# Kernel tuning notes

Measured on AMD Instinct MI355X. Metric: run time of the kernel, lower is better.

The kernel has to match this reference:

```python
import jax, jax.numpy as jnp
import numpy as np

VAR_FLOOR = 0.002
BS, A, IN, H, L, NNH, ATT, NACT = 1024, 32, 96, 64, 16, 64, 32, 16


def _lin(x, w, b):
    return x @ w.T + b


def _lrelu(x):
    return jax.nn.leaky_relu(x, 0.01)


def setup_inputs() -> dict:
    key = jax.random.key(0)
    ks = jax.random.split(key, 24)
    def w(k, o, i):
        return jax.random.normal(k, (o, i), jnp.float32) / np.float32(np.sqrt(i))
    def b(k, o):
        return jax.random.normal(k, (o,), jnp.float32) * 0.01
    N = BS * A
    return {
        "inputs": jax.random.normal(ks[0], (N, IN), jnp.float32),
        "hidden_state": jax.random.normal(ks[1], (N, H), jnp.float32),
        "eps": jax.random.normal(ks[2], (N, A * L), jnp.float32),
        "fc1_w": w(ks[3], H, IN), "fc1_b": b(ks[4], H),
        "gru_wih": w(ks[5], 3 * H, H), "gru_whh": w(ks[6], 3 * H, H),
        "gru_bih": b(ks[7], 3 * H), "gru_bhh": b(ks[8], 3 * H),
        "fc2_w": w(ks[9], NACT, H), "fc2_b": b(ks[10], NACT),
        "emb_w1": w(ks[11], NNH, H), "emb_b1": b(ks[12], NNH),
        "bn_g": jnp.ones((NNH,), jnp.float32), "bn_b": jnp.zeros((NNH,), jnp.float32),
        "emb_w2": w(ks[13], A * L * 2, NNH), "emb_b2": b(ks[14], A * L * 2),
        "msg_w1": w(ks[15], NNH, H + L), "msg_b1": b(ks[16], NNH),
        "msg_w2": w(ks[17], NACT, NNH), "msg_b2": b(ks[18], NACT),
        "wq_w": w(ks[19], ATT, H), "wq_b": b(ks[20], ATT),
        "wk_w": w(ks[21], ATT, L), "wk_b": b(ks[22], ATT),
        "bs": BS, "t": 0,
    }


def reference(inputs, hidden_state, eps, fc1_w, fc1_b, gru_wih, gru_whh, gru_bih,
              gru_bhh, fc2_w, fc2_b, emb_w1, emb_b1, bn_g, bn_b, emb_w2, emb_b2,
              msg_w1, msg_b1, msg_w2, msg_b2, wq_w, wq_b, wk_w, wk_b, bs, t):
    Hd = fc1_w.shape[0]
    x = jax.nn.relu(_lin(inputs, fc1_w, fc1_b))
    h_in = hidden_state.reshape(-1, Hd)
    # GRUCell
    gi = _lin(x, gru_wih, gru_bih)
    gh = _lin(h_in, gru_whh, gru_bhh)
    ir, iz, inn = jnp.split(gi, 3, axis=-1)
    hr, hz, hn = jnp.split(gh, 3, axis=-1)
    r = jax.nn.sigmoid(ir + hr)
    z = jax.nn.sigmoid(iz + hz)
    n = jnp.tanh(inn + r * hn)
    h = (1.0 - z) * n + z * h_in
    q = _lin(h, fc2_w, fc2_b)
    # embed_net: Linear -> BatchNorm(train) -> LeakyReLU -> Linear
    z1 = _lin(h, emb_w1, emb_b1)
    z1 = bn_g * (z1 - z1.mean(0)) / jnp.sqrt(z1.var(0) + 1e-5) + bn_b
    lat_par = _lin(_lrelu(z1), emb_w2, emb_b2)
    D = lat_par.shape[-1] // 2
    Ld = wk_w.shape[1]
    Ag = D // Ld
    mu = lat_par[:, :D]
    var = jnp.clip(jnp.exp(lat_par[:, D:]), VAR_FLOOR, None)
    latent = (mu + jnp.sqrt(var) * eps).reshape(bs, Ag, Ag, Ld)  # [b,i,j,L]
    # msg_net on (h of receiver j, latent[b,i,j])
    h3 = h.reshape(bs, Ag, Hd)
    h_rep = jnp.broadcast_to(h3[:, None, :, :], (bs, Ag, Ag, Hd))  # [b,i,j]=h[b,j]
    msg_in = jnp.concatenate([h_rep, latent], axis=-1)
    msg = _lin(_lrelu(_lin(msg_in, msg_w1, msg_b1)), msg_w2, msg_b2)  # (b,A,A,n_act)
    # attention gating
    att = wq_w.shape[0]
    query = _lin(h, wq_w, wq_b).reshape(bs, Ag, att) / np.float32(np.sqrt(att))
    key_ = _lin(latent, wk_w, wk_b)  # (b,A,A,att)
    alpha = jnp.einsum('bia,bija->bij', query, key_)
    alpha = jnp.where(jnp.eye(Ag, dtype=bool)[None], -1e9, alpha)
    alpha = jax.nn.softmax(alpha, axis=-1)
    agg = jnp.einsum('bij,bijn->bjn', alpha, msg)  # sum gated msgs over sender i
    return_q = q + agg.reshape(bs * Ag, -1)
    return (return_q, h)
```

## Files before the change

kernel.cpp:

```cpp
#include <hip/hip_runtime.h>
#include <math.h>

namespace {

constexpr int NROW = 32768;
constexpr int HDIM = 64;
constexpr int DH   = 512;

typedef __attribute__((ext_vector_type(8))) short bf16x8;
typedef __attribute__((ext_vector_type(4))) float f32x4;
typedef __attribute__((ext_vector_type(4))) unsigned uint4e;
typedef __attribute__((ext_vector_type(2))) unsigned uint2e;

__device__ __forceinline__ float sigmoidf_(float x) { return 1.f / (1.f + __expf(-x)); }
__device__ __forceinline__ float lrelu_(float x) { return x > 0.f ? x : 0.01f * x; }
__device__ __forceinline__ unsigned pkbf(float a, float b) {
  unsigned ua = __float_as_uint(a) + 0x8000u;
  unsigned ub = __float_as_uint(b) + 0x8000u;
  return __builtin_amdgcn_perm(ub, ua, 0x07060302);
}

__global__ __launch_bounds__(512, 1) void k_fgru(
    const float* __restrict__ in,
    const float* __restrict__ hprev,
    const float* __restrict__ fc1w, const float* __restrict__ fc1b,
    const float* __restrict__ wih, const float* __restrict__ whh,
    const float* __restrict__ bih, const float* __restrict__ bhh,
    const float* __restrict__ fc2w, const float* __restrict__ fc2b,
    const float* __restrict__ wqw, const float* __restrict__ wkw,
    const float* __restrict__ ew1, const float* __restrict__ eb1,
    float* __restrict__ qT, float* __restrict__ qkT, float* __restrict__ z1T,
    float* __restrict__ part, float* __restrict__ hout) {
  __shared__ char smem[91648];
  const int t = threadIdx.x;
  const int n0 = blockIdx.x * 128;
  short*    xS = (short*)smem;
  unsigned* gU = (unsigned*)(smem + 18432);
  float*    trF = (float*)(smem + 18432);
  unsigned* wU = (unsigned*)(smem + 73728);
  float*    sp1 = (float*)(smem + 87552);
  float*    sp2 = (float*)(smem + 89600);
  const float qs = 0.17677669529663687f;

  const float2* wih2 = (const float2*)wih;
  const float2* whh2 = (const float2*)whh;
  {
    float2 wv[12];
#pragma unroll
    for (int i = 0; i < 12; ++i) {
      int idx = t + 512 * i;
      int row = idx >> 5, kp = idx & 31;
      wv[i] = wih2[row * 32 + kp];
    }
#pragma unroll
    for (int i = 0; i < 12; ++i) {
      int idx = t + 512 * i;
      int row = idx >> 5, kp = idx & 31;
      int gate = row >> 6, cl = row & 63;
      gU[(gate * 64 + cl) * 36 + kp] = pkbf(wv[i].x, wv[i].y);
    }
#pragma unroll
    for (int i = 0; i < 12; ++i) {
      int idx = t + 512 * i;
      int row = idx >> 5, kp = idx & 31;
      wv[i] = whh2[row * 32 + kp];
    }
#pragma unroll
    for (int i = 0; i < 12; ++i) {
      int idx = t + 512 * i;
      int row = idx >> 5, kp = idx & 31;
      int gate = row >> 6, cl = row & 63;
      gU[((gate + 3) * 64 + cl) * 36 + kp] = pkbf(wv[i].x, wv[i].y);
    }
  }
  {
    float2 wv[5];
#pragma unroll
    for (int i = 0; i < 5; ++i) {
      int idx = t + 512 * i;
      int kp = idx & 31, cl = idx >> 5;
      const float* src = (cl < 16) ? (fc2w + cl * 64) : (ew1 + (cl - 16) * 64);
      wv[i] = *(const float2*)(src + 2 * kp);
    }
#pragma unroll
    for (int i = 0; i < 5; ++i) {
      int idx = t + 512 * i;
      int kp = idx & 31, cl = idx >> 5;
      int dst = (cl < 16) ? cl : (cl + 16);
      wU[dst * 36 + kp] = pkbf(wv[i].x, wv[i].y);
    }
  }
  {
    int kp = t & 31, row = t >> 5;
    float s0 = 0.f, s1 = 0.f;
#pragma unroll
    for (int a = 0; a < 32; ++a) {
      float wk = wkw[a * 16 + row];
      s0 = fmaf(wk, wqw[a * 64 + 2 * kp], s0);
      s1 = fmaf(wk, wqw[a * 64 + 2 * kp + 1], s1);
    }
    wU[(16 + row) * 36 + kp] = pkbf(s0 * qs, s1 * qs);
  }

  const int w = t >> 6, l = t & 63;
  const int m = l & 15, g = l >> 4;
  const int rowA = n0 + w * 16 + m;

  bf16x8 af[3];
#pragma unroll
  for (int ks = 0; ks < 3; ++ks) {
    const float4* p = (const float4*)(in + (size_t)rowA * 96 + ks * 32 + g * 8);
    float4 a = p[0], b = p[1];
    union { unsigned u[4]; bf16x8 h; } tw;
    tw.u[0] = pkbf(a.x, a.y); tw.u[1] = pkbf(a.z, a.w);
    tw.u[2] = pkbf(b.x, b.y); tw.u[3] = pkbf(b.z, b.w);
    af[ks] = tw.h;
  }
  {
    f32x4 accx[4];
#pragma unroll
    for (int ct = 0; ct < 4; ++ct) accx[ct] = (f32x4){0.f, 0.f, 0.f, 0.f};
#pragma unroll
    for (int ct = 0; ct < 4; ++ct)
#pragma unroll
      for (int ks = 0; ks < 3; ++ks) {
        const float4* p = (const float4*)(fc1w + (ct * 16 + m) * 96 + ks * 32 + g * 8);
        float4 a = p[0], b = p[1];
        union { unsigned u[4]; bf16x8 h; } tw;
        tw.u[0] = pkbf(a.x, a.y); tw.u[1] = pkbf(a.z, a.w);
        tw.u[2] = pkbf(b.x, b.y); tw.u[3] = pkbf(b.z, b.w);
        accx[ct] = __builtin_amdgcn_mfma_f32_16x16x32_bf16(af[ks], tw.h, accx[ct], 0, 0, 0);
      }
#pragma unroll
    for (int ct = 0; ct < 4; ++ct) {
      int c = ct * 16 + m;
      float bc = fc1b[c];
#pragma unroll
      for (int reg = 0; reg < 4; ++reg) {
        int nl = w * 16 + g * 4 + reg;
        float v = fmaxf(accx[ct][reg] + bc, 0.f);
        xS[nl * 72 + c] = (short)((__float_as_uint(v) + 0x8000u) >> 16);
      }
    }
  }
  __syncthreads();

  bf16x8 ax[2], ah[2];
#pragma unroll
  for (int ks = 0; ks < 2; ++ks) {
    ax[ks] = *(const bf16x8*)(xS + (w * 16 + m) * 72 + ks * 32 + g * 8);
    const float4* p = (const float4*)(hprev + (size_t)rowA * 64 + ks * 32 + g * 8);
    float4 a = p[0], b = p[1];
    union { unsigned u[4]; bf16x8 h; } tw;
    tw.u[0] = pkbf(a.x, a.y); tw.u[1] = pkbf(a.z, a.w);
    tw.u[2] = pkbf(b.x, b.y); tw.u[3] = pkbf(b.z, b.w);
    ah[ks] = tw.h;
  }
  const short* gS = (const short*)gU;
  float hc[4][4];
#pragma unroll 1
  for (int ct = 0; ct < 4; ++ct) {
    f32x4 a_ir = (f32x4){0.f,0.f,0.f,0.f}, a_iz = (f32x4){0.f,0.f,0.f,0.f},
          a_in = (f32x4){0.f,0.f,0.f,0.f}, a_hr = (f32x4){0.f,0.f,0.f,0.f},
          a_hz = (f32x4){0.f,0.f,0.f,0.f}, a_hn = (f32x4){0.f,0.f,0.f,0.f};
    int crow = ct * 16 + m;
#pragma unroll
    for (int ks = 0; ks < 2; ++ks) {
      bf16x8 b0 = *(const bf16x8*)(gS + (0 * 64 + crow) * 72 + ks * 32 + g * 8);
      bf16x8 b1 = *(const bf16x8*)(gS + (1 * 64 + crow) * 72 + ks * 32 + g * 8);
      bf16x8 b2 = *(const bf16x8*)(gS + (2 * 64 + crow) * 72 + ks * 32 + g * 8);
      bf16x8 b3 = *(const bf16x8*)(gS + (3 * 64 + crow) * 72 + ks * 32 + g * 8);
      bf16x8 b4 = *(const bf16x8*)(gS + (4 * 64 + crow) * 72 + ks * 32 + g * 8);
      bf16x8 b5 = *(const bf16x8*)(gS + (5 * 64 + crow) * 72 + ks * 32 + g * 8);
      a_ir = __builtin_amdgcn_mfma_f32_16x16x32_bf16(ax[ks], b0, a_ir, 0, 0, 0);
      a_iz = __builtin_amdgcn_mfma_f32_16x16x32_bf16(ax[ks], b1, a_iz, 0, 0, 0);
      a_in = __builtin_amdgcn_mfma_f32_16x16x32_bf16(ax[ks], b2, a_in, 0, 0, 0);
      a_hr = __builtin_amdgcn_mfma_f32_16x16x32_bf16(ah[ks], b3, a_hr, 0, 0, 0);
      a_hz = __builtin_amdgcn_mfma_f32_16x16x32_bf16(ah[ks], b4, a_hz, 0, 0, 0);
      a_hn = __builtin_amdgcn_mfma_f32_16x16x32_bf16(ah[ks], b5, a_hn, 0, 0, 0);
    }
    float bir = bih[crow], biz = bih[64 + crow], bin = bih[128 + crow];
    float bhr = bhh[crow], bhz = bhh[64 + crow], bhn = bhh[128 + crow];
#pragma unroll
    for (int reg = 0; reg < 4; ++reg) {
      int nl = w * 16 + g * 4 + reg;
      float hv = hprev[(size_t)(n0 + nl) * 64 + crow];
      float r  = sigmoidf_(a_ir[reg] + bir + a_hr[reg] + bhr);
      float z  = sigmoidf_(a_iz[reg] + biz + a_hz[reg] + bhz);
      float nn = tanhf(a_in[reg] + bin + r * (a_hn[reg] + bhn));
      hc[ct][reg] = (1.f - z) * nn + z * hv;
    }
  }
#pragma unroll
  for (int ct = 0; ct < 4; ++ct)
#pragma unroll
    for (int reg = 0; reg < 4; ++reg) {
      int nl = w * 16 + g * 4 + reg;
      xS[nl * 72 + ct * 16 + m] =
          (short)((__float_as_uint(hc[ct][reg]) + 0x8000u) >> 16);
    }

  bf16x8 af2[2];
#pragma unroll
  for (int ks = 0; ks < 2; ++ks)
    af2[ks] = *(const bf16x8*)(xS + (w * 16 + m) * 72 + ks * 32 + g * 8);
  const short* sW = (const short*)wU;
  f32x4 acc[6];
#pragma unroll
  for (int ct = 0; ct < 6; ++ct) acc[ct] = (f32x4){0.f, 0.f, 0.f, 0.f};
#pragma unroll
  for (int ct = 0; ct < 6; ++ct)
#pragma unroll
    for (int ks = 0; ks < 2; ++ks) {
      bf16x8 bw = *(const bf16x8*)(sW + (ct * 16 + m) * 72 + ks * 32 + g * 8);
      acc[ct] = __builtin_amdgcn_mfma_f32_16x16x32_bf16(af2[ks], bw, acc[ct], 0, 0, 0);
    }

  __syncthreads();
#pragma unroll
  for (int ct = 0; ct < 4; ++ct)
#pragma unroll
    for (int reg = 0; reg < 4; ++reg)
      trF[(ct * 16 + m) * 133 + w * 16 + g * 4 + reg] = hc[ct][reg];
  __syncthreads();
#pragma unroll
  for (int i = 0; i < 16; ++i) {
    int idx = t + 512 * i;
    int c = idx & 63, nl = idx >> 6;
    hout[(size_t)(n0 + nl) * 64 + c] = trF[c * 133 + nl];
  }

  float s1[4], s2[4];
#pragma unroll
  for (int zt = 0; zt < 4; ++zt) { s1[zt] = 0.f; s2[zt] = 0.f; }
  {
    int nb = n0 + w * 16 + g * 4;
    {
      float bc = fc2b[m];
      f32x4 v;
#pragma unroll
      for (int reg = 0; reg < 4; ++reg) v[reg] = acc[0][reg] + bc;
      *(f32x4*)(qT + (size_t)m * NROW + nb) = v;
    }
    *(f32x4*)(qkT + (size_t)m * NROW + nb) = acc[1];
#pragma unroll
    for (int ct = 2; ct < 6; ++ct) {
      int z = (ct - 2) * 16 + m;
      float bc = eb1[z];
      f32x4 v;
#pragma unroll
      for (int reg = 0; reg < 4; ++reg) {
        float zv = acc[ct][reg] + bc;
        v[reg] = zv;
        s1[ct - 2] += zv;
        s2[ct - 2] = fmaf(zv, zv, s2[ct - 2]);
      }
      *(f32x4*)(z1T + (size_t)z * NROW + nb) = v;
    }
  }
#pragma unroll
  for (int zt = 0; zt < 4; ++zt) {
    s1[zt] += __shfl_down(s1[zt], 16, 64);
    s1[zt] += __shfl_down(s1[zt], 32, 64);
    s2[zt] += __shfl_down(s2[zt], 16, 64);
    s2[zt] += __shfl_down(s2[zt], 32, 64);
  }
  if (l < 16) {
#pragma unroll
    for (int zt = 0; zt < 4; ++zt) {
      sp1[w * 64 + zt * 16 + m] = s1[zt];
      sp2[w * 64 + zt * 16 + m] = s2[zt];
    }
  }
  __syncthreads();
  if (t < 64) {
    float a1 = 0.f, a2 = 0.f;
#pragma unroll
    for (int k = 0; k < 8; ++k) {
      a1 += sp1[k * 64 + t];
      a2 += sp2[k * 64 + t];
    }
    part[(size_t)blockIdx.x * 128 + t] = a1;
    part[(size_t)blockIdx.x * 128 + 64 + t] = a2;
  }
}

__global__ __launch_bounds__(256) void k_bnstat(const float* __restrict__ part,
    const float* __restrict__ bng, const float* __restrict__ bnb,
    const float* __restrict__ ew2,
    float* __restrict__ stat, unsigned* __restrict__ ew2b) {
  if (blockIdx.x == 0) {
    __shared__ float red[512];
    const int t = threadIdx.x;
    const int c = t & 63, q = t >> 6;
    float s1 = 0.f, s2 = 0.f;
#pragma unroll 4
    for (int b = q; b < 256; b += 4) {
      s1 += part[(size_t)b * 128 + c];
      s2 += part[(size_t)b * 128 + 64 + c];
    }
    red[q * 64 + c] = s1;
    red[256 + q * 64 + c] = s2;
    __syncthreads();
    if (t < 64) {
      float a1 = red[t] + red[64 + t] + red[128 + t] + red[192 + t];
      float a2 = red[256 + t] + red[320 + t] + red[384 + t] + red[448 + t];
      float mean = a1 * (1.f / NROW);
      float var = a2 * (1.f / NROW) - mean * mean;
      float rstd = rsqrtf(var + 1e-5f);
      float sc = bng[t] * rstd;
      stat[t] = sc;
      stat[64 + t] = bnb[t] - mean * sc;
    }
  } else {
    const int rb = blockIdx.x - 1;
    const int t = threadIdx.x;
#pragma unroll
    for (int it = 0; it < 2; ++it) {
      int id2 = t + 256 * it;
      int r = rb * 16 + (id2 >> 5);
      int cp = id2 & 31;
      float2 v = *(const float2*)(ew2 + (size_t)r * 64 + 2 * cp);
      ew2b[(size_t)r * 32 + cp] = pkbf(v.x, v.y);
    }
  }
}

constexpr int LATB_OFF = 0;
constexpr int H3B_OFF  = 36864;
constexpr int W1H_OFF  = 41728;
constexpr int W1L_OFF  = 51456;
constexpr int W2P_OFF  = 54016;
constexpr int ALL_OFF  = 56448;
constexpr int MT_OFF   = 60672;
constexpr int QKL_OFF  = MT_OFF + 4864;
__global__ __launch_bounds__(512, 1) void k_msg(
    const unsigned* __restrict__ ew2b, const float* __restrict__ stat,
    const float* __restrict__ z1T, const float* __restrict__ eb2,
    const float* __restrict__ eps,
    const float* __restrict__ qkT,
    const float* __restrict__ qT, const float* __restrict__ hrow,
    const float* __restrict__ w1, const float* __restrict__ b1,
    const float* __restrict__ w2, const float* __restrict__ b2,
    float* __restrict__ out) {
  __shared__ char smem[81152];
  const int t = threadIdx.x;
  const int b = blockIdx.x;
  const int b32 = b * 32;
  unsigned* latB_dw = (unsigned*)(smem + LATB_OFF);

  const int w = t >> 6, l = t & 63;
  const int m = l & 15, g = l >> 4;

  {
    short* xz = (short*)(smem + MT_OFF);
    float zv[4];
#pragma unroll
    for (int it = 0; it < 4; ++it) {
      int idx = t + 512 * it;
      int i = idx & 31, c = idx >> 5;
      zv[it] = z1T[(size_t)c * NROW + b32 + i];
    }
#pragma unroll
    for (int it = 0; it < 4; ++it) {
      int idx = t + 512 * it;
      int i = idx & 31, c = idx >> 5;
      float v = lrelu_(fmaf(stat[c], zv[it], stat[64 + c]));
      xz[i * 76 + c] = (short)((__float_as_uint(v) + 0x8000u) >> 16);
    }
  }
  {
    float* qkL = (float*)(smem + QKL_OFF);
    int i = t & 31, ll = t >> 5;
    qkL[i * 20 + ll] = qkT[(size_t)ll * NROW + b32 + i];
  }
  {
    int cp = t & 31, jbase = t >> 5;
    const float2* h2 = (const float2*)hrow;
    float2 hv[2];
#pragma unroll
    for (int it = 0; it < 2; ++it)
      hv[it] = h2[((size_t)(b32 + jbase + 16 * it) * 64 + 2 * cp) >> 1];
    unsigned* dst = (unsigned*)(smem + H3B_OFF);
#pragma unroll
    for (int it = 0; it < 2; ++it)
      dst[(jbase + 16 * it) * 38 + cp] = pkbf(hv[it].x, hv[it].y);
  }
  {
    int kp = t & 31, cb = t >> 5;
    const float2* w12 = (const float2*)w1;
    float2 wv[4];
#pragma unroll
    for (int it = 0; it < 4; ++it)
      wv[it] = w12[((cb + 16 * it) * 80 + 2 * kp) >> 1];
    unsigned* dst = (unsigned*)(smem + W1H_OFF);
#pragma unroll
    for (int it = 0; it < 4; ++it)
      dst[(cb + 16 * it) * 38 + kp] = pkbf(wv[it].x, wv[it].y);
  }
  {
    int lp = t & 7, cc = t >> 3;
    const float2* w12 = (const float2*)w1;
    float2 wv = w12[(cc * 80 + 64 + 2 * lp) >> 1];
    unsigned* dst = (unsigned*)(smem + W1L_OFF);
    dst[cc * 10 + lp] = pkbf(wv.x, wv.y);
  }
  {
    int pp = t & 31, nn = t >> 5;
    const float2* w22 = (const float2*)w2;
    int p = 2 * pp;
    int c = ((p >> 2) & 3) * 16 + (p >> 4) * 4 + (p & 3);
    float2 wv0 = w22[(nn * 64 + c) >> 1];
    unsigned* dst = (unsigned*)(smem + W2P_OFF);
    dst[nn * 38 + pp] = pkbf(wv0.x, wv0.y);
  }
  __syncthreads();

  {
    const short* xzS = (const short*)(smem + MT_OFF);
    bf16x8 afz[2][2];
#pragma unroll
    for (int mt = 0; mt < 2; ++mt)
#pragma unroll
      for (int ks = 0; ks < 2; ++ks)
        afz[mt][ks] = *(const bf16x8*)(xzS + (mt * 16 + m) * 76 + ks * 32 + g * 8);
    const uint4e* w4 = (const uint4e*)ew2b;
    const float stdfloor = 0.04472135955f;

    union { uint4e u; bf16x8 h; } bmuC[2], blvC[2], bmuN[2], blvN[2];
    float epC[2][4], epN[2][4];
    {
      int ci = w * 4;
#pragma unroll
      for (int ks = 0; ks < 2; ++ks) {
        bmuC[ks].u = w4[(size_t)(ci * 16 + m) * 8 + ks * 4 + g];
        blvC[ks].u = w4[(size_t)(512 + ci * 16 + m) * 8 + ks * 4 + g];
      }
#pragma unroll
      for (int mt = 0; mt < 2; ++mt)
#pragma unroll
        for (int reg = 0; reg < 4; ++reg)
          epC[mt][reg] = eps[(size_t)(b32 + mt * 16 + g * 4 + reg) * 512 + ci * 16 + m];
    }
#pragma unroll
    for (int ci8 = 0; ci8 < 4; ++ci8) {
      int ci = w * 4 + ci8;
      int c = ci * 16 + m;
      if (ci8 < 3) {
        int ciN = ci + 1;
#pragma unroll
        for (int ks = 0; ks < 2; ++ks) {
          bmuN[ks].u = w4[(size_t)(ciN * 16 + m) * 8 + ks * 4 + g];
          blvN[ks].u = w4[(size_t)(512 + ciN * 16 + m) * 8 + ks * 4 + g];
        }
#pragma unroll
        for (int mt = 0; mt < 2; ++mt)
#pragma unroll
          for (int reg = 0; reg < 4; ++reg)
            epN[mt][reg] = eps[(size_t)(b32 + mt * 16 + g * 4 + reg) * 512 + ciN * 16 + m];
      }
      f32x4 accm[2], accl[2];
#pragma unroll
      for (int mt = 0; mt < 2; ++mt) {
        accm[mt] = (f32x4){0.f, 0.f, 0.f, 0.f};
        accl[mt] = (f32x4){0.f, 0.f, 0.f, 0.f};
      }
#pragma unroll
      for (int ks = 0; ks < 2; ++ks)
#pragma unroll
        for (int mt = 0; mt < 2; ++mt) {
          accm[mt] = __builtin_amdgcn_mfma_f32_16x16x32_bf16(afz[mt][ks], bmuC[ks].h, accm[mt], 0, 0, 0);
          accl[mt] = __builtin_amdgcn_mfma_f32_16x16x32_bf16(afz[mt][ks], blvC[ks].h, accl[mt], 0, 0, 0);
        }
      float ebm = eb2[c], ebl = eb2[DH + c];
#pragma unroll
      for (int mt = 0; mt < 2; ++mt)
#pragma unroll
        for (int reg = 0; reg < 4; ++reg) {
          float mu = accm[mt][reg] + ebm;
          float lv = accl[mt][reg] + ebl;
          float sd = fmaxf(__expf(0.5f * lv), stdfloor);
          float lat = fmaf(sd, epC[mt][reg], mu);
          float lat2 = __shfl_xor(lat, 1, 64);
          if (!(m & 1)) {
            int i = mt * 16 + g * 4 + reg;
            latB_dw[(i * 32 + (ci ^ g)) * 9 + (m >> 1)] = pkbf(lat, lat2);
          }
        }
      if (ci8 < 3) {
#pragma unroll
        for (int ks = 0; ks < 2; ++ks) { bmuC[ks].u = bmuN[ks].u; blvC[ks].u = blvN[ks].u; }
#pragma unroll
        for (int mt = 0; mt < 2; ++mt)
#pragma unroll
          for (int reg = 0; reg < 4; ++reg) epC[mt][reg] = epN[mt][reg];
      }
    }
  }
  __syncthreads();

  {
    const float* qkL = (const float*)(smem + QKL_OFF);
    float* alL = (float*)(smem + ALL_OFF);
#pragma unroll 1
    for (int p = 0; p < 2; ++p) {
      int i = (t >> 5) + 16 * p;
      int j = t & 31;
      int sw = (i >> 2) & 3;
      const unsigned* lr = latB_dw + (i * 32 + (j ^ sw)) * 9;
      float acc = 0.f;
#pragma unroll
      for (int d = 0; d < 8; ++d) {
        unsigned u = lr[d];
        float lo = __uint_as_float(u << 16);
        float hi = __uint_as_float(u & 0xffff0000u);
        acc = fmaf(lo, qkL[i * 20 + 2 * d], acc);
        acc = fmaf(hi, qkL[i * 20 + 2 * d + 1], acc);
      }
      if (j == i) acc = -1e9f;
      float mx = acc;
#pragma unroll
      for (int msk = 16; msk > 0; msk >>= 1) mx = fmaxf(mx, __shfl_xor(mx, msk, 32));
      float e = __expf(acc - mx);
      float s = e;
#pragma unroll
      for (int msk = 16; msk > 0; msk >>= 1) s += __shfl_xor(s, msk, 32);
      alL[i * 33 + j] = e / s;
    }
  }

  const int n15 = l & 15, q = l >> 4;
  const int jh = w & 1, ibase = (w >> 1) * 8;
  const bool kact = (q < 2);

  f32x4 hp[4];
#pragma unroll
  for (int ct = 0; ct < 4; ++ct) hp[ct] = (f32x4){0.f, 0.f, 0.f, 0.f};
#pragma unroll
  for (int ct = 0; ct < 4; ++ct)
#pragma unroll
    for (int ks = 0; ks < 2; ++ks) {
      bf16x8 aF = *(const bf16x8*)(smem + W1H_OFF + (ct * 16 + n15) * 152 + ks * 64 + q * 16);
      bf16x8 bF = *(const bf16x8*)(smem + H3B_OFF + (jh * 16 + n15) * 152 + ks * 64 + q * 16);
      hp[ct] = __builtin_amdgcn_mfma_f32_16x16x32_bf16(aF, bF, hp[ct], 0, 0, 0);
    }
#pragma unroll
  for (int ct = 0; ct < 4; ++ct)
#pragma unroll
    for (int reg = 0; reg < 4; ++reg)
      hp[ct][reg] += b1[ct * 16 + q * 4 + reg];

  bf16x8 aL[4];
#pragma unroll
  for (int ct = 0; ct < 4; ++ct) {
    union { unsigned u[4]; bf16x8 h; } tmp;
    tmp.u[0] = tmp.u[1] = tmp.u[2] = tmp.u[3] = 0u;
    if (kact) {
      const unsigned* p = (const unsigned*)(smem + W1L_OFF) + (ct * 16 + n15) * 10 + q * 4;
      uint2e d0 = *(const uint2e*)p;
      uint2e d1 = *(const uint2e*)(p + 2);
      tmp.u[0] = d0.x; tmp.u[1] = d0.y; tmp.u[2] = d1.x; tmp.u[3] = d1.y;
    }
    aL[ct] = tmp.h;
  }
  bf16x8 w2F[2];
#pragma unroll
  for (int ks = 0; ks < 2; ++ks)
    w2F[ks] = *(const bf16x8*)(smem + W2P_OFF + n15 * 152 + ks * 64 + q * 16);
  float b2v[4];
#pragma unroll
  for (int reg = 0; reg < 4; ++reg) b2v[reg] = b2[q * 4 + reg];

  __syncthreads();

  float agg[4] = {0.f, 0.f, 0.f, 0.f};
  char* wb = smem + MT_OFF + w * 2560;
  const float* alLf = (const float*)(smem + ALL_OFF);
#pragma unroll 1
  for (int it = 0; it < 8; ++it) {
    int ii = ibase + it;
    int sw = (ii >> 2) & 3;
    int r = ii * 32 + jh * 16 + (n15 ^ sw);
    union { unsigned u[4]; bf16x8 h; } latF;
    latF.u[0] = latF.u[1] = latF.u[2] = latF.u[3] = 0u;
    if (kact) {
      const unsigned* p = latB_dw + r * 9 + q * 4;
      latF.u[0] = p[0]; latF.u[1] = p[1]; latF.u[2] = p[2]; latF.u[3] = p[3];
    }
    f32x4 acc[4];
#pragma unroll
    for (int ct = 0; ct < 4; ++ct) {
      acc[ct] = (f32x4){0.f, 0.f, 0.f, 0.f};
      acc[ct] = __builtin_amdgcn_mfma_f32_16x16x32_bf16(aL[ct], latF.h, acc[ct], 0, 0, 0);
    }
#pragma unroll
    for (int h = 0; h < 2; ++h) {
      float m0[4], m1[4];
#pragma unroll
      for (int reg = 0; reg < 4; ++reg) {
        float v0 = acc[2 * h][reg] + hp[2 * h][reg];
        float v1 = acc[2 * h + 1][reg] + hp[2 * h + 1][reg];
        m0[reg] = fmaxf(v0, 0.01f * v0);
        m1[reg] = fmaxf(v1, 0.01f * v1);
      }
      uint4e pk4;
      pk4.x = pkbf(m0[0], m0[1]); pk4.y = pkbf(m0[2], m0[3]);
      pk4.z = pkbf(m1[0], m1[1]); pk4.w = pkbf(m1[2], m1[3]);
      int qp = (2 * q + h) & 3;
      *(uint4e*)(wb + (q >> 1) * 1280 + n15 * 80 + qp * 16) = pk4;
    }
    f32x4 msg = (f32x4){0.f, 0.f, 0.f, 0.f};
#pragma unroll
    for (int ks = 0; ks < 2; ++ks) {
      bf16x8 mF = *(const bf16x8*)(wb + ks * 1280 + n15 * 80 + q * 16);
      msg = __builtin_amdgcn_mfma_f32_16x16x32_bf16(w2F[ks], mF, msg, 0, 0, 0);
    }
    float aw = alLf[ii * 33 + jh * 16 + n15];
#pragma unroll
    for (int reg = 0; reg < 4; ++reg)
      agg[reg] = fmaf(aw, msg[reg] + b2v[reg], agg[reg]);
  }
  {
    f32x4 av; av[0] = agg[0]; av[1] = agg[1]; av[2] = agg[2]; av[3] = agg[3];
    *(f32x4*)(wb + n15 * 80 + q * 16) = av;
  }
  __syncthreads();
  {
    int jg = t >> 4, nn = t & 15;
    int jh2 = jg >> 4, jl = jg & 15;
    float s = qT[(size_t)nn * NROW + b32 + jg];
#pragma unroll
    for (int k = 0; k < 4; ++k)
      s += *(const float*)(smem + MT_OFF + (jh2 + 2 * k) * 2560 + jl * 80 + nn * 4);
    out[(size_t)b * 512 + t] = s;
  }
}

}

extern "C" void kernel_launch(void* const* d_in, const int* in_sizes, int n_in,
                              void* d_out, int out_size, void* d_ws, size_t ws_size,
                              hipStream_t stream) {
  (void)in_sizes; (void)n_in; (void)out_size; (void)ws_size;
  const float* inputs = (const float*)d_in[0];
  const float* hidden = (const float*)d_in[1];
  const float* eps    = (const float*)d_in[2];
  const float* fc1w   = (const float*)d_in[3];
  const float* fc1b   = (const float*)d_in[4];
  const float* wih    = (const float*)d_in[5];
  const float* whh    = (const float*)d_in[6];
  const float* bih    = (const float*)d_in[7];
  const float* bhh    = (const float*)d_in[8];
  const float* fc2w   = (const float*)d_in[9];
  const float* fc2b   = (const float*)d_in[10];
  const float* ew1    = (const float*)d_in[11];
  const float* eb1    = (const float*)d_in[12];
  const float* bng    = (const float*)d_in[13];
  const float* bnb    = (const float*)d_in[14];
  const float* ew2    = (const float*)d_in[15];
  const float* eb2    = (const float*)d_in[16];
  const float* w1     = (const float*)d_in[17];
  const float* b1     = (const float*)d_in[18];
  const float* w2     = (const float*)d_in[19];
  const float* b2     = (const float*)d_in[20];
  const float* wqw    = (const float*)d_in[21];
  const float* wkw    = (const float*)d_in[23];

  float* ws = (float*)d_ws;
  float* qT     = ws + 2097152;
  float* qkT    = ws + 2621440;
  float* z1T    = ws + 3670016;
  float* part   = ws + 5767168;
  float* stat   = ws + 5832704;
  unsigned* ew2b = (unsigned*)(ws + 5832832);

  float* out_q = (float*)d_out;
  float* out_h = (float*)d_out + 524288;

  hipLaunchKernelGGL(k_fgru, dim3(256), dim3(512), 0, stream,
                     inputs, hidden, fc1w, fc1b, wih, whh, bih, bhh,
                     fc2w, fc2b, wqw, wkw, ew1, eb1,
                     qT, qkT, z1T, part, out_h);
  hipLaunchKernelGGL(k_bnstat, dim3(65), dim3(256), 0, stream, part, bng, bnb, ew2, stat, ew2b);
  hipLaunchKernelGGL(k_msg, dim3(1024), dim3(512), 0, stream,
                     ew2b, stat, z1T, eb2, eps, qkT, qT, out_h, w1, b1, w2, b2, out_q);
}
```

Measured before the change: 212.7 us.

## Read GRU weights from global instead of LDS and raise occupancy

The GRU input and hidden weight matrices are no longer converted to bf16 and staged in shared memory. Each wave now loads and packs its weight fragments straight from global memory, relying on cache hits. This cuts the LDS footprint so more blocks fit per CU, raises the launch bound, and moves a few barriers since the transpose buffer gets its own region. The cost is repeated global/L2 weight traffic and per-wave conversion work inside the gate loop.

New measurement: 227.0 us. +6.7%, slower.

```diff
diff --git a/kernel.cpp b/kernel.cpp
--- a/kernel.cpp
+++ b/kernel.cpp
@@ -19,8 +19,16 @@
   unsigned ub = __float_as_uint(b) + 0x8000u;
   return __builtin_amdgcn_perm(ub, ua, 0x07060302);
 }
-
-__global__ __launch_bounds__(512, 1) void k_fgru(
+__device__ __forceinline__ bf16x8 ldpk(const float* base) {
+  const float4* p = (const float4*)base;
+  float4 a = p[0], b = p[1];
+  union { unsigned u[4]; bf16x8 h; } tw;
+  tw.u[0] = pkbf(a.x, a.y); tw.u[1] = pkbf(a.z, a.w);
+  tw.u[2] = pkbf(b.x, b.y); tw.u[3] = pkbf(b.z, b.w);
+  return tw.h;
+}
+
+__global__ __launch_bounds__(512, 4) void k_fgru(
     const float* __restrict__ in,
     const float* __restrict__ hprev,
     const float* __restrict__ fc1w, const float* __restrict__ fc1b,
@@ -31,48 +39,16 @@
     const float* __restrict__ ew1, const float* __restrict__ eb1,
     float* __restrict__ qT, float* __restrict__ qkT, float* __restrict__ z1T,
     float* __restrict__ part, float* __restrict__ hout) {
-  __shared__ char smem[91648];
+  __shared__ char smem[70400];
   const int t = threadIdx.x;
   const int n0 = blockIdx.x * 128;
   short*    xS = (short*)smem;
-  unsigned* gU = (unsigned*)(smem + 18432);
-  float*    trF = (float*)(smem + 18432);
-  unsigned* wU = (unsigned*)(smem + 73728);
-  float*    sp1 = (float*)(smem + 87552);
-  float*    sp2 = (float*)(smem + 89600);
+  unsigned* wU = (unsigned*)(smem + 18432);
+  float*    trF = (float*)(smem + 32256);
+  float*    sp1 = (float*)(smem + 66304);
+  float*    sp2 = (float*)(smem + 68352);
   const float qs = 0.17677669529663687f;
 
-  const float2* wih2 = (const float2*)wih;
-  const float2* whh2 = (const float2*)whh;
-  {
-    float2 wv[12];
-#pragma unroll
-    for (int i = 0; i < 12; ++i) {
-      int idx = t + 512 * i;
-      int row = idx >> 5, kp = idx & 31;
-      wv[i] = wih2[row * 32 + kp];
-    }
-#pragma unroll
-    for (int i = 0; i < 12; ++i) {
-      int idx = t + 512 * i;
-      int row = idx >> 5, kp = idx & 31;
-      int gate = row >> 6, cl = row & 63;
-      gU[(gate * 64 + cl) * 36 + kp] = pkbf(wv[i].x, wv[i].y);
-    }
-#pragma unroll
-    for (int i = 0; i < 12; ++i) {
-      int idx = t + 512 * i;
-      int row = idx >> 5, kp = idx & 31;
-      wv[i] = whh2[row * 32 + kp];
-    }
-#pragma unroll
-    for (int i = 0; i < 12; ++i) {
-      int idx = t + 512 * i;
-      int row = idx >> 5, kp = idx & 31;
-      int gate = row >> 6, cl = row & 63;
-      gU[((gate + 3) * 64 + cl) * 36 + kp] = pkbf(wv[i].x, wv[i].y);
-    }
-  }
   {
     float2 wv[5];
 #pragma unroll
@@ -108,14 +84,8 @@
 
   bf16x8 af[3];
 #pragma unroll
-  for (int ks = 0; ks < 3; ++ks) {
-    const float4* p = (const float4*)(in + (size_t)rowA * 96 + ks * 32 + g * 8);
-    float4 a = p[0], b = p[1];
-    union { unsigned u[4]; bf16x8 h; } tw;
-    tw.u[0] = pkbf(a.x, a.y); tw.u[1] = pkbf(a.z, a.w);
-    tw.u[2] = pkbf(b.x, b.y); tw.u[3] = pkbf(b.z, b.w);
-    af[ks] = tw.h;
-  }
+  for (int ks = 0; ks < 3; ++ks)
+    af[ks] = ldpk(in + (size_t)rowA * 96 + ks * 32 + g * 8);
   {
     f32x4 accx[4];
 #pragma unroll
@@ -124,12 +94,8 @@
     for (int ct = 0; ct < 4; ++ct)
 #pragma unroll
       for (int ks = 0; ks < 3; ++ks) {
-        const float4* p = (const float4*)(fc1w + (ct * 16 + m) * 96 + ks * 32 + g * 8);
-        float4 a = p[0], b = p[1];
-        union { unsigned u[4]; bf16x8 h; } tw;
-        tw.u[0] = pkbf(a.x, a.y); tw.u[1] = pkbf(a.z, a.w);
-        tw.u[2] = pkbf(b.x, b.y); tw.u[3] = pkbf(b.z, b.w);
-        accx[ct] = __builtin_amdgcn_mfma_f32_16x16x32_bf16(af[ks], tw.h, accx[ct], 0, 0, 0);
+        bf16x8 bw = ldpk(fc1w + (ct * 16 + m) * 96 + ks * 32 + g * 8);
+        accx[ct] = __builtin_amdgcn_mfma_f32_16x16x32_bf16(af[ks], bw, accx[ct], 0, 0, 0);
       }
 #pragma unroll
     for (int ct = 0; ct < 4; ++ct) {
@@ -143,20 +109,13 @@
       }
     }
   }
-  __syncthreads();
 
   bf16x8 ax[2], ah[2];
 #pragma unroll
   for (int ks = 0; ks < 2; ++ks) {
     ax[ks] = *(const bf16x8*)(xS + (w * 16 + m) * 72 + ks * 32 + g * 8);
-    const float4* p = (const float4*)(hprev + (size_t)rowA * 64 + ks * 32 + g * 8);
-    float4 a = p[0], b = p[1];
-    union { unsigned u[4]; bf16x8 h; } tw;
-    tw.u[0] = pkbf(a.x, a.y); tw.u[1] = pkbf(a.z, a.w);
-    tw.u[2] = pkbf(b.x, b.y); tw.u[3] = pkbf(b.z, b.w);
-    ah[ks] = tw.h;
-  }
-  const short* gS = (const short*)gU;
+    ah[ks] = ldpk(hprev + (size_t)rowA * 64 + ks * 32 + g * 8);
+  }
   float hc[4][4];
 #pragma unroll 1
   for (int ct = 0; ct < 4; ++ct) {
@@ -166,12 +125,14 @@
     int crow = ct * 16 + m;
 #pragma unroll
     for (int ks = 0; ks < 2; ++ks) {
-      bf16x8 b0 = *(const bf16x8*)(gS + (0 * 64 + crow) * 72 + ks * 32 + g * 8);
-      bf16x8 b1 = *(const bf16x8*)(gS + (1 * 64 + crow) * 72 + ks * 32 + g * 8);
-      bf16x8 b2 = *(const bf16x8*)(gS + (2 * 64 + crow) * 72 + ks * 32 + g * 8);
-      bf16x8 b3 = *(const bf16x8*)(gS + (3 * 64 + crow) * 72 + ks * 32 + g * 8);
-      bf16x8 b4 = *(const bf16x8*)(gS + (4 * 64 + crow) * 72 + ks * 32 + g * 8);
-      bf16x8 b5 = *(const bf16x8*)(gS + (5 * 64 + crow) * 72 + ks * 32 + g * 8);
+      const float* wb_ = wih + (size_t)crow * 64 + ks * 32 + g * 8;
+      const float* hb_ = whh + (size_t)crow * 64 + ks * 32 + g * 8;
+      bf16x8 b0 = ldpk(wb_);
+      bf16x8 b1 = ldpk(wb_ + 64 * 64);
+      bf16x8 b2 = ldpk(wb_ + 128 * 64);
+      bf16x8 b3 = ldpk(hb_);
+      bf16x8 b4 = ldpk(hb_ + 64 * 64);
+      bf16x8 b5 = ldpk(hb_ + 128 * 64);
       a_ir = __builtin_amdgcn_mfma_f32_16x16x32_bf16(ax[ks], b0, a_ir, 0, 0, 0);
       a_iz = __builtin_amdgcn_mfma_f32_16x16x32_bf16(ax[ks], b1, a_iz, 0, 0, 0);
       a_in = __builtin_amdgcn_mfma_f32_16x16x32_bf16(ax[ks], b2, a_in, 0, 0, 0);
@@ -199,6 +160,7 @@
       xS[nl * 72 + ct * 16 + m] =
           (short)((__float_as_uint(hc[ct][reg]) + 0x8000u) >> 16);
     }
+  __syncthreads();
 
   bf16x8 af2[2];
 #pragma unroll
@@ -216,7 +178,6 @@
       acc[ct] = __builtin_amdgcn_mfma_f32_16x16x32_bf16(af2[ks], bw, acc[ct], 0, 0, 0);
     }
 
-  __syncthreads();
 #pragma unroll
   for (int ct = 0; ct < 4; ++ct)
 #pragma unroll
```
